# Kernel optimization log

Measured on AMD Instinct MI355X. Metric: run time of the kernel, lower is better.

The kernel has to match this reference:

```python
import jax, jax.numpy as jnp
import numpy as np
from jax import lax

NUM_ITERATIONS = 200  # matches num_iterations=200 in the torch module
MAX_DET = 100         # fixed max number of boxes per image (jit-static)


def setup_inputs() -> dict:
    key = jax.random.key(0)
    B, C, H, W = 32, 1, 512, 512
    # uint8-range image; after /255 and >0.5 threshold ~half the pixels are foreground
    image = jax.random.randint(key, (B, C, H, W), 0, 256).astype(jnp.float32)
    return {"image": image}


def _batch_mask_to_boxes(image, num_iterations, max_det):
    x = image / 255.0                      # the module's image.div(255.0)
    mask = x[:, 0] > 0.5                   # [B,H,W] foreground mask
    B, H, W = mask.shape
    HW = H * W
    m_i = mask.astype(jnp.int32)

    # unique positive label per foreground pixel, 0 = background
    labels0 = jnp.arange(1, HW + 1, dtype=jnp.int32).reshape(1, H, W) * m_i

    # connected components via iterative 3x3 max-pool label propagation
    def step(lab, _):
        lab = lax.reduce_window(lab, jnp.int32(0), lax.max,
                                (1, 3, 3), (1, 1, 1), "SAME") * m_i
        return lab, None

    labels, _ = lax.scan(step, labels0, None, length=num_iterations)

    # per-(image, label) bounding boxes via segment reductions
    seg = labels.reshape(B, HW) + (jnp.arange(B, dtype=jnp.int32) * (HW + 1))[:, None]
    seg = seg.reshape(-1)                                             # [B*HW]
    rows = jnp.broadcast_to(jnp.arange(H, dtype=jnp.float32)[None, :, None], (B, H, W)).reshape(-1)
    cols = jnp.broadcast_to(jnp.arange(W, dtype=jnp.float32)[None, None, :], (B, H, W)).reshape(-1)
    nseg = B * (HW + 1)
    ymin = jax.ops.segment_min(rows, seg, num_segments=nseg)
    ymax = jax.ops.segment_max(rows, seg, num_segments=nseg)
    xmin = jax.ops.segment_min(cols, seg, num_segments=nseg)
    xmax = jax.ops.segment_max(cols, seg, num_segments=nseg)
    counts = jax.ops.segment_sum(jnp.ones_like(rows), seg, num_segments=nseg)

    counts = counts.reshape(B, HW + 1).at[:, 0].set(0.0)  # drop background
    boxes_all = jnp.stack([xmin, ymin, xmax, ymax], axis=-1).reshape(B, HW + 1, 4)

    # keep the max_det largest components per image (fixed output shape)
    top_counts, top_idx = lax.top_k(counts, max_det)                  # [B,max_det]
    boxes = jnp.take_along_axis(boxes_all, top_idx[:, :, None], axis=1)  # [B,max_det,4]
    valid = (top_counts > 0.0)[:, :, None]
    return jnp.where(valid, boxes, 0.0)


def reference(image):
    return _batch_mask_to_boxes(image, NUM_ITERATIONS, MAX_DET)
```

## Files before the change

kernel.cpp:

```cpp
#include <hip/hip_runtime.h>
#include <cstdint>

#define IW 512
#define IH 512
#define HW 262144
#define NIMG 32
#define MAXD 100
#define TH 48
#define HALO 8
#define CX 112
#define CY 32
#define NPASS 25
#define NTX 5
#define NTY 16
#define GH 32768
#define SLOTS 2048
#define DCAP 8192
#define CAP 8192

#define OFF_LABB  33554688ull
#define OFF_DLIST 25165824ull
#define OFF_SMALL 26214400ull

__device__ __forceinline__ int imax3(int a, int b, int c) {
    int m = a > b ? a : b;
    return m > c ? m : c;
}

__global__ __launch_bounds__(256) void init_labels(const float4* __restrict__ img,
                                                   int4* __restrict__ lab) {
    const size_t n = (size_t)NIMG * HW / 4;
    const size_t stride = (size_t)gridDim.x * 256;
    for (size_t i = (size_t)blockIdx.x * 256 + threadIdx.x; i < n; i += stride) {
        float4 f = img[i];
        int p = (int)((i * 4) & (HW - 1));
        int4 o;
        o.x = (f.x > 127.5f) ? p + 1 : 0;
        o.y = (f.y > 127.5f) ? p + 2 : 0;
        o.z = (f.z > 127.5f) ? p + 3 : 0;
        o.w = (f.w > 127.5f) ? p + 4 : 0;
        lab[i] = o;
    }
}

__global__ __launch_bounds__(64) void prop_pass(const int* __restrict__ in,
                                                int* __restrict__ out) {
    const int img = blockIdx.z;
    const int x0 = blockIdx.x * CX - HALO;
    const int y0 = blockIdx.y * CY - HALO;
    const int lane = threadIdx.x;
    const int xe = x0 + 2 * lane;
    const bool colok = (xe >= 0) && (xe < IW);
    const int2* __restrict__ ip2 = (const int2*)(in + (size_t)img * HW);
    int2* __restrict__ op2 = (int2*)(out + (size_t)img * HW);

    int a[TH], b[TH];
#pragma unroll
    for (int i = 0; i < TH; ++i) {
        int gy = y0 + i;
        int2 ld = make_int2(0, 0);
        if (colok && gy >= 0 && gy < IH) ld = ip2[gy * (IW / 2) + (xe >> 1)];
        a[i] = ld.x; b[i] = ld.y;
    }

#pragma unroll 1
    for (int it = 0; it < HALO; ++it) {
        int la0 = __shfl_up(b[0], 1, 64);
        int ra0 = __shfl_down(a[0], 1, 64);
        int haP = 0, hbP = 0;
        int haC = imax3(la0, a[0], b[0]);
        int hbC = imax3(a[0], b[0], ra0);
#pragma unroll
        for (int i = 0; i < TH; ++i) {
            int haN = 0, hbN = 0;
            if (i < TH - 1) {
                int l = __shfl_up(b[i + 1], 1, 64);
                int r = __shfl_down(a[i + 1], 1, 64);
                haN = imax3(l, a[i + 1], b[i + 1]);
                hbN = imax3(a[i + 1], b[i + 1], r);
            }
            int na = imax3(haP, haC, haN);
            int nb = imax3(hbP, hbC, hbN);
            a[i] = (a[i] == 0) ? 0 : na;
            b[i] = (b[i] == 0) ? 0 : nb;
            haP = haC; haC = haN; hbP = hbC; hbC = hbN;
        }
    }

    if (lane >= 4 && lane < 60 && colok) {
#pragma unroll
        for (int i = HALO; i < TH - HALO; ++i) {
            int gy = y0 + i;
            if (gy < IH) op2[gy * (IW / 2) + (xe >> 1)] = make_int2(a[i], b[i]);
        }
    }
}

__device__ __forceinline__ unsigned gfind_ins(unsigned* __restrict__ gk, unsigned key,
                                              unsigned* __restrict__ dlist,
                                              unsigned* __restrict__ dcount) {
    unsigned h = (key * 2654435761u) >> 17;
    for (unsigned pr = 0; pr < GH; ++pr) {
        unsigned idx = (h + pr) & (GH - 1);
        unsigned k = gk[idx];
        if (k == key) return idx;
        if (k == 0u) {
            unsigned old = atomicCAS(&gk[idx], 0u, key);
            if (old == 0u) {
                unsigned pos = atomicAdd(dcount, 1u);
                if (pos < DCAP) dlist[pos] = idx;
                return idx;
            }
            if (old == key) return idx;
        }
    }
    return h;
}

__global__ __launch_bounds__(256) void stat_pass(const int* __restrict__ lab,
                                                 unsigned* __restrict__ gk,
                                                 unsigned* __restrict__ gcnt,
                                                 unsigned* __restrict__ gx0,
                                                 unsigned* __restrict__ gx1,
                                                 unsigned* __restrict__ gy0,
                                                 unsigned* __restrict__ gy1,
                                                 unsigned* __restrict__ dlist,
                                                 unsigned* __restrict__ dcount) {
    __shared__ unsigned hk[SLOTS], hc[SLOTS];
    __shared__ unsigned sx0[SLOTS], sx1[SLOTS], sy0[SLOTS], sy1[SLOTS];
    const int img = blockIdx.y;
    const int rb = blockIdx.x * 16;
    const int t = threadIdx.x;
    for (int i = t; i < SLOTS; i += 256) {
        hk[i] = 0; hc[i] = 0;
        sx0[i] = 0xFFFFFFFFu; sy0[i] = 0xFFFFFFFFu; sx1[i] = 0; sy1[i] = 0;
    }
    __syncthreads();
    unsigned* gki = gk + (size_t)img * GH;
    unsigned* gci = gcnt + (size_t)img * GH;
    unsigned* gx0i = gx0 + (size_t)img * GH;
    unsigned* gx1i = gx1 + (size_t)img * GH;
    unsigned* gy0i = gy0 + (size_t)img * GH;
    unsigned* gy1i = gy1 + (size_t)img * GH;
    unsigned* dli = dlist + (size_t)img * DCAP;
    unsigned* dci = dcount + img;

    const int4* lp = (const int4*)(lab + (size_t)img * HW + rb * IW);
    for (int i = t; i < 16 * IW / 4; i += 256) {
        int4 v = lp[i];
        unsigned y = (unsigned)(rb + (i >> 7));
        unsigned xb = (unsigned)((i & 127) << 2);
        int larr[4] = {v.x, v.y, v.z, v.w};
#pragma unroll
        for (int e = 0; e < 4; ++e) {
            unsigned l = (unsigned)larr[e];
            if (!l) continue;
            unsigned x = xb + (unsigned)e;
            unsigned h = (l * 2654435761u) >> 21;
            int idx = -1;
            for (int pr = 0; pr < 32; ++pr) {
                unsigned j = (h + pr) & (SLOTS - 1);
                unsigned k = hk[j];
                if (k == l) { idx = (int)j; break; }
                if (k == 0u) {
                    unsigned old = atomicCAS(&hk[j], 0u, l);
                    if (old == 0u || old == l) { idx = (int)j; break; }
                }
            }
            if (idx >= 0) {
                atomicAdd(&hc[idx], 1u);
                atomicMin(&sx0[idx], x); atomicMax(&sx1[idx], x);
                atomicMin(&sy0[idx], y); atomicMax(&sy1[idx], y);
            } else {
                unsigned g = gfind_ins(gki, l, dli, dci);
                atomicAdd(&gci[g], 1u);
                atomicMin(&gx0i[g], x); atomicMax(&gx1i[g], x);
                atomicMin(&gy0i[g], y); atomicMax(&gy1i[g], y);
            }
        }
    }
    __syncthreads();
    for (int i = t; i < SLOTS; i += 256) {
        unsigned k = hk[i];
        if (!k) continue;
        unsigned g = gfind_ins(gki, k, dli, dci);
        atomicAdd(&gci[g], hc[i]);
        atomicMin(&gx0i[g], sx0[i]); atomicMax(&gx1i[g], sx1[i]);
        atomicMin(&gy0i[g], sy0[i]); atomicMax(&gy1i[g], sy1[i]);
    }
}

__global__ __launch_bounds__(256) void topk(const unsigned* __restrict__ gk,
                                            const unsigned* __restrict__ gcnt,
                                            const unsigned* __restrict__ dlist,
                                            const unsigned* __restrict__ dcount,
                                            unsigned* __restrict__ rank_count,
                                            unsigned* __restrict__ rank_slot) {
    __shared__ unsigned long long keys[CAP];
    __shared__ unsigned long long wred[4];
    const int img = blockIdx.x;
    const int t = threadIdx.x;
    const int lane = t & 63, wid = t >> 6;
    for (int i = t; i < CAP; i += 256) keys[i] = 0;
    __syncthreads();

    unsigned nd = dcount[img];
    if (nd > CAP) nd = CAP;
    const unsigned* gki = gk + (size_t)img * GH;
    const unsigned* gci = gcnt + (size_t)img * GH;
    const unsigned* dli = dlist + (size_t)img * DCAP;
    for (unsigned i = t; i < nd; i += 256) {
        unsigned slot = dli[i];
        unsigned lb = gki[slot];
        unsigned c = gci[slot];
        keys[i] = ((((unsigned long long)c << 19) | (unsigned)(HW - lb)) << 15)
                  | slot;
    }
    __syncthreads();

    unsigned long long maxv = 0; int maxi = -1;
    for (int i = t; i < CAP; i += 256) {
        unsigned long long k = keys[i];
        if (k > maxv) { maxv = k; maxi = i; }
    }

    for (int r = 0; r < MAXD; ++r) {
        unsigned long long m = maxv;
        for (int s = 1; s < 64; s <<= 1) {
            unsigned long long o = (unsigned long long)__shfl_xor((long long)m, s, 64);
            if (o > m) m = o;
        }
        if (lane == 0) wred[wid] = m;
        __syncthreads();
        unsigned long long w = wred[0];
        if (wred[1] > w) w = wred[1];
        if (wred[2] > w) w = wred[2];
        if (wred[3] > w) w = wred[3];
        if (w != 0ull && maxv == w) {
            keys[maxi] = 0;
            rank_count[img * MAXD + r] = (unsigned)(w >> 34);
            rank_slot[img * MAXD + r]  = (unsigned)(w & 32767ull);
            maxv = 0; maxi = -1;
            for (int i = t; i < CAP; i += 256) {
                unsigned long long k = keys[i];
                if (k > maxv) { maxv = k; maxi = i; }
            }
        }
        if (w == 0ull && t == 0) {
            rank_count[img * MAXD + r] = 0;
            rank_slot[img * MAXD + r] = 0;
        }
        __syncthreads();
    }
}

__global__ __launch_bounds__(256) void final_out(const unsigned* __restrict__ rank_count,
                                                 const unsigned* __restrict__ rank_slot,
                                                 const unsigned* __restrict__ gx0,
                                                 const unsigned* __restrict__ gx1,
                                                 const unsigned* __restrict__ gy0,
                                                 const unsigned* __restrict__ gy1,
                                                 float* __restrict__ out) {
    int id = blockIdx.x * 256 + threadIdx.x;
    if (id >= NIMG * MAXD) return;
    unsigned c = rank_count[id];
    float4 b = make_float4(0.f, 0.f, 0.f, 0.f);
    if (c) {
        int img = id / MAXD;
        size_t g = (size_t)img * GH + rank_slot[id];
        b = make_float4((float)gx0[g], (float)gy0[g], (float)gx1[g], (float)gy1[g]);
    }
    reinterpret_cast<float4*>(out)[id] = b;
}

extern "C" void kernel_launch(void* const* d_in, const int* in_sizes, int n_in,
                              void* d_out, int out_size, void* d_ws, size_t ws_size,
                              hipStream_t stream) {
    (void)in_sizes; (void)n_in; (void)out_size; (void)ws_size;
    const float* img = (const float*)d_in[0];
    char* ws = (char*)d_ws;

    int* labA = (int*)ws;
    int* labB = (int*)(ws + OFF_LABB);
    unsigned* gk   = (unsigned*)ws;
    unsigned* gcnt = (unsigned*)(ws + 4194304ull);
    unsigned* gx1  = (unsigned*)(ws + 8388608ull);
    unsigned* gy1  = (unsigned*)(ws + 12582912ull);
    unsigned* gx0  = (unsigned*)(ws + 16777216ull);
    unsigned* gy0  = (unsigned*)(ws + 20971520ull);
    unsigned* dlist = (unsigned*)(ws + OFF_DLIST);
    unsigned* dcount = (unsigned*)(ws + OFF_SMALL);
    unsigned* rank_count = (unsigned*)(ws + OFF_SMALL + 128ull);
    unsigned* rank_slot  = (unsigned*)(ws + OFF_SMALL + 128ull + 16384ull);
    float* out = (float*)d_out;

    init_labels<<<2048, 256, 0, stream>>>((const float4*)img, (int4*)labA);

    dim3 pg(NTX, NTY, NIMG);
    const int* pin = labA; int* pout = labB;
    for (int p = 0; p < NPASS; ++p) {
        prop_pass<<<pg, 64, 0, stream>>>(pin, pout);
        int* tmp = (int*)pin; pin = pout; pout = tmp;
    }

    hipMemsetAsync(gk, 0, 16777216ull, stream);
    hipMemsetAsync(gx0, 0xFF, 8388608ull, stream);
    hipMemsetAsync(dcount, 0, 128ull, stream);

    stat_pass<<<dim3(32, NIMG), 256, 0, stream>>>(pin, gk, gcnt, gx0, gx1, gy0, gy1,
                                                  dlist, dcount);
    topk<<<NIMG, 256, 0, stream>>>(gk, gcnt, dlist, dcount, rank_count, rank_slot);
    final_out<<<(NIMG * MAXD + 255) / 256, 256, 0, stream>>>(rank_count, rank_slot,
                                                             gx0, gx1, gy0, gy1, out);
}
```

Before: 1.531 ms.

## Shrink global hash table, merge label runs with wave-level aggregation, retile propagation

```diff
diff --git a/kernel.cpp b/kernel.cpp
--- a/kernel.cpp
+++ b/kernel.cpp
@@ -6,26 +6,28 @@
 #define HW 262144
 #define NIMG 32
 #define MAXD 100
-#define TH 48
+#define TH 40
 #define HALO 8
 #define CX 112
-#define CY 32
+#define CY 24
 #define NPASS 25
 #define NTX 5
-#define NTY 16
-#define GH 32768
+#define NTY 22
+#define GH 8192
 #define SLOTS 2048
 #define DCAP 8192
 #define CAP 8192
 
 #define OFF_LABB  33554688ull
-#define OFF_DLIST 25165824ull
-#define OFF_SMALL 26214400ull
+#define OFF_DLIST 6295552ull
+#define OFF_SMALL 8388608ull
 
 __device__ __forceinline__ int imax3(int a, int b, int c) {
     int m = a > b ? a : b;
     return m > c ? m : c;
 }
+__device__ __forceinline__ unsigned umin2(unsigned a, unsigned b) { return a < b ? a : b; }
+__device__ __forceinline__ unsigned umax2(unsigned a, unsigned b) { return a > b ? a : b; }
 
 __global__ __launch_bounds__(256) void init_labels(const float4* __restrict__ img,
                                                    int4* __restrict__ lab) {
@@ -99,7 +101,7 @@
 __device__ __forceinline__ unsigned gfind_ins(unsigned* __restrict__ gk, unsigned key,
                                               unsigned* __restrict__ dlist,
                                               unsigned* __restrict__ dcount) {
-    unsigned h = (key * 2654435761u) >> 17;
+    unsigned h = (key * 2654435761u) >> 19;
     for (unsigned pr = 0; pr < GH; ++pr) {
         unsigned idx = (h + pr) & (GH - 1);
         unsigned k = gk[idx];
@@ -120,64 +122,88 @@
 __global__ __launch_bounds__(256) void stat_pass(const int* __restrict__ lab,
                                                  unsigned* __restrict__ gk,
                                                  unsigned* __restrict__ gcnt,
-                                                 unsigned* __restrict__ gx0,
+                                                 unsigned* __restrict__ gx0r,
                                                  unsigned* __restrict__ gx1,
-                                                 unsigned* __restrict__ gy0,
+                                                 unsigned* __restrict__ gy0r,
                                                  unsigned* __restrict__ gy1,
                                                  unsigned* __restrict__ dlist,
                                                  unsigned* __restrict__ dcount) {
     __shared__ unsigned hk[SLOTS], hc[SLOTS];
-    __shared__ unsigned sx0[SLOTS], sx1[SLOTS], sy0[SLOTS], sy1[SLOTS];
+    __shared__ unsigned sx0r[SLOTS], sx1[SLOTS], sy0r[SLOTS], sy1[SLOTS];
     const int img = blockIdx.y;
     const int rb = blockIdx.x * 16;
     const int t = threadIdx.x;
+    const int lane = t & 63;
     for (int i = t; i < SLOTS; i += 256) {
-        hk[i] = 0; hc[i] = 0;
-        sx0[i] = 0xFFFFFFFFu; sy0[i] = 0xFFFFFFFFu; sx1[i] = 0; sy1[i] = 0;
+        hk[i] = 0; hc[i] = 0; sx0r[i] = 0; sx1[i] = 0; sy0r[i] = 0; sy1[i] = 0;
     }
     __syncthreads();
     unsigned* gki = gk + (size_t)img * GH;
     unsigned* gci = gcnt + (size_t)img * GH;
-    unsigned* gx0i = gx0 + (size_t)img * GH;
+    unsigned* gx0i = gx0r + (size_t)img * GH;
     unsigned* gx1i = gx1 + (size_t)img * GH;
-    unsigned* gy0i = gy0 + (size_t)img * GH;
+    unsigned* gy0i = gy0r + (size_t)img * GH;
     unsigned* gy1i = gy1 + (size_t)img * GH;
     unsigned* dli = dlist + (size_t)img * DCAP;
     unsigned* dci = dcount + img;
+
+    auto upd = [&](unsigned l, unsigned cnt, unsigned x0, unsigned x1, unsigned y) {
+        unsigned h = (l * 2654435761u) >> 21;
+        int idx = -1;
+        for (int pr = 0; pr < 32; ++pr) {
+            unsigned j = (h + pr) & (SLOTS - 1);
+            unsigned k = hk[j];
+            if (k == l) { idx = (int)j; break; }
+            if (k == 0u) {
+                unsigned old = atomicCAS(&hk[j], 0u, l);
+                if (old == 0u || old == l) { idx = (int)j; break; }
+            }
+        }
+        if (idx >= 0) {
+            atomicAdd(&hc[idx], cnt);
+            atomicMax(&sx0r[idx], 511u - x0); atomicMax(&sx1[idx], x1);
+            atomicMax(&sy0r[idx], 511u - y);  atomicMax(&sy1[idx], y);
+        } else {
+            unsigned g = gfind_ins(gki, l, dli, dci);
+            atomicAdd(&gci[g], cnt);
+            atomicMax(&gx0i[g], 511u - x0); atomicMax(&gx1i[g], x1);
+            atomicMax(&gy0i[g], 511u - y);  atomicMax(&gy1i[g], y);
+        }
+    };
 
     const int4* lp = (const int4*)(lab + (size_t)img * HW + rb * IW);
     for (int i = t; i < 16 * IW / 4; i += 256) {
         int4 v = lp[i];
         unsigned y = (unsigned)(rb + (i >> 7));
         unsigned xb = (unsigned)((i & 127) << 2);
-        int larr[4] = {v.x, v.y, v.z, v.w};
-#pragma unroll
-        for (int e = 0; e < 4; ++e) {
-            unsigned l = (unsigned)larr[e];
-            if (!l) continue;
-            unsigned x = xb + (unsigned)e;
-            unsigned h = (l * 2654435761u) >> 21;
-            int idx = -1;
-            for (int pr = 0; pr < 32; ++pr) {
-                unsigned j = (h + pr) & (SLOTS - 1);
-                unsigned k = hk[j];
-                if (k == l) { idx = (int)j; break; }
-                if (k == 0u) {
-                    unsigned old = atomicCAS(&hk[j], 0u, l);
-                    if (old == 0u || old == l) { idx = (int)j; break; }
-                }
-            }
-            if (idx >= 0) {
-                atomicAdd(&hc[idx], 1u);
-                atomicMin(&sx0[idx], x); atomicMax(&sx1[idx], x);
-                atomicMin(&sy0[idx], y); atomicMax(&sy1[idx], y);
-            } else {
-                unsigned g = gfind_ins(gki, l, dli, dci);
-                atomicAdd(&gci[g], 1u);
-                atomicMin(&gx0i[g], x); atomicMax(&gx1i[g], x);
-                atomicMin(&gy0i[g], y); atomicMax(&gy1i[g], y);
-            }
-        }
+        unsigned l0 = (unsigned)v.x, l1 = (unsigned)v.y,
+                 l2 = (unsigned)v.z, l3 = (unsigned)v.w;
+        unsigned rep = l0 ? l0 : (l1 ? l1 : (l2 ? l2 : l3));
+        unsigned long long actm = __ballot(rep != 0u);
+        if (actm == 0ull) continue;
+        int src = __ffsll((long long)actm) - 1;
+        unsigned maj = (unsigned)__shfl((int)rep, src, 64);
+
+        unsigned mcnt = 0, mx0 = 0xFFFFu, mx1 = 0;
+#define EMIT(L, A, B)                                                          \
+        if (L) {                                                               \
+            if ((L) == maj) { mcnt += (B) - (A) + 1;                           \
+                mx0 = umin2(mx0, xb + (A)); mx1 = umax2(mx1, xb + (B)); }      \
+            else upd((L), (B) - (A) + 1, xb + (A), xb + (B), y);               \
+        }
+        unsigned cur = l0; unsigned rx0 = 0;
+        if (l1 != cur) { EMIT(cur, rx0, 0u); cur = l1; rx0 = 1; }
+        if (l2 != cur) { EMIT(cur, rx0, 1u); cur = l2; rx0 = 2; }
+        if (l3 != cur) { EMIT(cur, rx0, 2u); cur = l3; rx0 = 3; }
+        EMIT(cur, rx0, 3u);
+#undef EMIT
+        for (int s = 1; s < 64; s <<= 1) {
+            mcnt += (unsigned)__shfl_xor((int)mcnt, s, 64);
+            unsigned o0 = (unsigned)__shfl_xor((int)mx0, s, 64);
+            unsigned o1 = (unsigned)__shfl_xor((int)mx1, s, 64);
+            mx0 = umin2(mx0, o0); mx1 = umax2(mx1, o1);
+        }
+        if (lane == src && mcnt > 0) upd(maj, mcnt, mx0, mx1, y);
     }
     __syncthreads();
     for (int i = t; i < SLOTS; i += 256) {
@@ -185,8 +211,8 @@
         if (!k) continue;
         unsigned g = gfind_ins(gki, k, dli, dci);
         atomicAdd(&gci[g], hc[i]);
-        atomicMin(&gx0i[g], sx0[i]); atomicMax(&gx1i[g], sx1[i]);
-        atomicMin(&gy0i[g], sy0[i]); atomicMax(&gy1i[g], sy1[i]);
+        atomicMax(&gx0i[g], sx0r[i]); atomicMax(&gx1i[g], sx1[i]);
+        atomicMax(&gy0i[g], sy0r[i]); atomicMax(&gy1i[g], sy1[i]);
     }
 }
 
@@ -256,9 +282,9 @@
 
 __global__ __launch_bounds__(256) void final_out(const unsigned* __restrict__ rank_count,
                                                  const unsigned* __restrict__ rank_slot,
-                                                 const unsigned* __restrict__ gx0,
+                                                 const unsigned* __restrict__ gx0r,
                                                  const unsigned* __restrict__ gx1,
-                                                 const unsigned* __restrict__ gy0,
+                                                 const unsigned* __restrict__ gy0r,
                                                  const unsigned* __restrict__ gy1,
                                                  float* __restrict__ out) {
     int id = blockIdx.x * 256 + threadIdx.x;
@@ -268,7 +294,8 @@
     if (c) {
         int img = id / MAXD;
         size_t g = (size_t)img * GH + rank_slot[id];
-        b = make_float4((float)gx0[g], (float)gy0[g], (float)gx1[g], (float)gy1[g]);
+        b = make_float4((float)(511u - gx0r[g]), (float)(511u - gy0r[g]),
+                        (float)gx1[g], (float)gy1[g]);
     }
     reinterpret_cast<float4*>(out)[id] = b;
 }
@@ -283,15 +310,15 @@
     int* labA = (int*)ws;
     int* labB = (int*)(ws + OFF_LABB);
     unsigned* gk   = (unsigned*)ws;
-    unsigned* gcnt = (unsigned*)(ws + 4194304ull);
-    unsigned* gx1  = (unsigned*)(ws + 8388608ull);
-    unsigned* gy1  = (unsigned*)(ws + 12582912ull);
-    unsigned* gx0  = (unsigned*)(ws + 16777216ull);
-    unsigned* gy0  = (unsigned*)(ws + 20971520ull);
+    unsigned* gcnt = (unsigned*)(ws + 1048576ull);
+    unsigned* gx1  = (unsigned*)(ws + 2097152ull);
+    unsigned* gy1  = (unsigned*)(ws + 3145728ull);
+    unsigned* gx0r = (unsigned*)(ws + 4194304ull);
+    unsigned* gy0r = (unsigned*)(ws + 5242880ull);
+    unsigned* dcount = (unsigned*)(ws + 6291456ull);
     unsigned* dlist = (unsigned*)(ws + OFF_DLIST);
-    unsigned* dcount = (unsigned*)(ws + OFF_SMALL);
-    unsigned* rank_count = (unsigned*)(ws + OFF_SMALL + 128ull);
-    unsigned* rank_slot  = (unsigned*)(ws + OFF_SMALL + 128ull + 16384ull);
+    unsigned* rank_count = (unsigned*)(ws + OFF_SMALL);
+    unsigned* rank_slot  = (unsigned*)(ws + OFF_SMALL + 16384ull);
     float* out = (float*)d_out;
 
     init_labels<<<2048, 256, 0, stream>>>((const float4*)img, (int4*)labA);
@@ -303,13 +330,11 @@
         int* tmp = (int*)pin; pin = pout; pout = tmp;
     }
 
-    hipMemsetAsync(gk, 0, 16777216ull, stream);
-    hipMemsetAsync(gx0, 0xFF, 8388608ull, stream);
-    hipMemsetAsync(dcount, 0, 128ull, stream);
-
-    stat_pass<<<dim3(32, NIMG), 256, 0, stream>>>(pin, gk, gcnt, gx0, gx1, gy0, gy1,
+    hipMemsetAsync(gk, 0, 6291456ull + 4096ull, stream);
+
+    stat_pass<<<dim3(32, NIMG), 256, 0, stream>>>(pin, gk, gcnt, gx0r, gx1, gy0r, gy1,
                                                   dlist, dcount);
     topk<<<NIMG, 256, 0, stream>>>(gk, gcnt, dlist, dcount, rank_count, rank_slot);
     final_out<<<(NIMG * MAXD + 255) / 256, 256, 0, stream>>>(rank_count, rank_slot,
-                                                             gx0, gx1, gy0, gy1, out);
-}
+                                                             gx0r, gx1, gy0r, gy1, out);
+}
```

After: 1.727 ms. 12.8% more time.
